# Kernel tuning notes

Hardware: AMD Instinct MI355X
Metric: run time of the kernel (lower is better)

Reference implementation:

```python
import jax, jax.numpy as jnp
import numpy as np
from functools import partial

D, H, O = 4, 64, 2  # input_dim, hidden_dim, output_dim


def lstm_layer(x, Wih, Whh, bih, bhh):
    """Single PyTorch-convention LSTM layer. x: [B,T,Din] -> [B,T,H].
    Gate order i,f,g,o; weights Wih:[4H,Din], Whh:[4H,H]."""
    B = x.shape[0]
    Hd = Whh.shape[1]
    # precompute input contribution for all timesteps (one big GEMM)
    xg = jnp.einsum('btd,gd->btg', x, Wih) + bih + bhh  # [B,T,4H]

    def step(carry, xg_t):
        h, c = carry
        g = xg_t + h @ Whh.T  # [B,4H]
        i, f, gg, o = jnp.split(g, 4, axis=-1)
        i = jax.nn.sigmoid(i)
        f = jax.nn.sigmoid(f)
        gg = jnp.tanh(gg)
        o = jax.nn.sigmoid(o)
        c = f * c + i * gg
        h = o * jnp.tanh(c)
        return (h, c), h

    h0 = jnp.zeros((B, Hd), x.dtype)
    c0 = jnp.zeros((B, Hd), x.dtype)
    (_, _), hs = jax.lax.scan(step, (h0, c0), jnp.swapaxes(xg, 0, 1))  # hs: [T,B,H]
    return jnp.swapaxes(hs, 0, 1)


def setup_inputs() -> dict:
    key = jax.random.key(0)
    ks = jax.random.split(key, 13)
    s_ih0 = 1.0 / np.sqrt(H)
    inp = {
        'x': jax.random.normal(ks[0], (16384, 100, D), jnp.float32),
        'W_ih0': jax.random.uniform(ks[1], (4 * H, D), jnp.float32, -s_ih0, s_ih0),
        'W_hh0': jax.random.uniform(ks[2], (4 * H, H), jnp.float32, -s_ih0, s_ih0),
        'b_ih0': jax.random.uniform(ks[3], (4 * H,), jnp.float32, -s_ih0, s_ih0),
        'b_hh0': jax.random.uniform(ks[4], (4 * H,), jnp.float32, -s_ih0, s_ih0),
        'W_ih1': jax.random.uniform(ks[5], (4 * H, H), jnp.float32, -s_ih0, s_ih0),
        'W_hh1': jax.random.uniform(ks[6], (4 * H, H), jnp.float32, -s_ih0, s_ih0),
        'b_ih1': jax.random.uniform(ks[7], (4 * H,), jnp.float32, -s_ih0, s_ih0),
        'b_hh1': jax.random.uniform(ks[8], (4 * H,), jnp.float32, -s_ih0, s_ih0),
        'gamma': jnp.ones((H,), jnp.float32),
        'beta': jnp.zeros((H,), jnp.float32),
        'W_fc': jax.random.uniform(ks[9], (O, H), jnp.float32, -s_ih0, s_ih0),
        'b_fc': jax.random.uniform(ks[10], (O,), jnp.float32, -s_ih0, s_ih0),
    }
    return inp


def reference(x, W_ih0, W_hh0, b_ih0, b_hh0, W_ih1, W_hh1, b_ih1, b_hh1,
              gamma, beta, W_fc, b_fc):
    h1 = lstm_layer(x, W_ih0, W_hh0, b_ih0, b_hh0)   # [B,T,H]
    h2 = lstm_layer(h1, W_ih1, W_hh1, b_ih1, b_hh1)  # [B,T,H] (dropout off: eval)
    last = h2[:, -1, :]                              # [B,H]
    mu = jnp.mean(last, axis=-1, keepdims=True)
    var = jnp.mean((last - mu) ** 2, axis=-1, keepdims=True)
    normed = (last - mu) * jax.lax.rsqrt(var + 1e-5) * gamma + beta
    return normed @ W_fc.T + b_fc                    # [B,2]
```

## Files before the change

kernel.cpp:

```cpp
#include <hip/hip_runtime.h>

#define TSTEPS 100
#define BC     16
#define NBLK   (16384/BC)

typedef __attribute__((ext_vector_type(8))) short bf16x8;
typedef __attribute__((ext_vector_type(4))) short s16x4;
typedef __attribute__((ext_vector_type(4))) float f32x4;
typedef __attribute__((ext_vector_type(2))) float f32x2;

#define WS_WHH0_U 0
#define WS_WIH1_U 16384
#define WS_WHH1_U 32768
#define WS_WIH0_U 49152
#define WS_B0_F   28672
#define WS_B1_F   28928
#define WS_XF_U   65536
#define WS_NEED   (131072 + (size_t)NBLK * TSTEPS * 64 * 2)

#define MFMA(A,B,C) __builtin_amdgcn_mfma_f32_16x16x32_bf16(A,B,C,0,0,0)
#define LOG2E 1.4426950408889634f
#define BF16_ONE ((short)0x3F80)

__device__ __forceinline__ unsigned short f2bf_rne(float f) {
    unsigned int u = __float_as_uint(f);
    u += 0x7fffu + ((u >> 16) & 1u);
    return (unsigned short)(u >> 16);
}
__device__ __forceinline__ unsigned short f2bf(float f) {
    return (unsigned short)((__float_as_uint(f) + 0x8000u) >> 16);
}
__device__ __forceinline__ f32x2 exp2v(f32x2 y) {
    return (f32x2){__builtin_amdgcn_exp2f(y.x), __builtin_amdgcn_exp2f(y.y)};
}
__device__ __forceinline__ f32x2 rcpv(f32x2 y) {
    return (f32x2){__builtin_amdgcn_rcpf(y.x), __builtin_amdgcn_rcpf(y.y)};
}

__device__ __forceinline__ f32x2 lstm_cell(f32x2 yi, f32x2 yf, f32x2 yg, f32x2 yo,
                                           f32x2& c) {
    const f32x2 one = {1.f, 1.f};
    const f32x2 L22 = {2.0f * LOG2E, 2.0f * LOG2E};
    const f32x2 Ei = exp2v(yi), Ef = exp2v(yf), Eg = exp2v(yg), Eo = exp2v(yo);
    const f32x2 t2 = Ef + one;
    const f32x2 t3 = Eg + one;
    const f32x2 u  = Ei * t3 + t3;
    const f32x2 n  = Eg * t2 - t2;
    const f32x2 R1 = rcpv(u * t2);
    c = (c * u + n) * R1;
    const f32x2 Ec = exp2v(c * L22);
    const f32x2 t6 = Ec + one;
    const f32x2 R2 = rcpv(Eo * t6 + t6);
    return Ec * R2 - R2;
}

__device__ __forceinline__ void bar_lds() {
    asm volatile("s_waitcnt lgkmcnt(0)\n\ts_barrier" ::: "memory");
}

__global__ void reorder_w(const float* __restrict__ Wih0, const float* __restrict__ Whh0,
                          const float* __restrict__ bih0, const float* __restrict__ bhh0,
                          const float* __restrict__ Wih1, const float* __restrict__ Whh1,
                          const float* __restrict__ bih1, const float* __restrict__ bhh1,
                          unsigned short* __restrict__ wsu, float* __restrict__ wsf)
{
    const int idx = blockIdx.x * 256 + threadIdx.x;
    if (idx < 16384) {
        const int j = idx & 7, lane = (idx >> 3) & 63, kc = (idx >> 9) & 1,
                  G = (idx >> 10) & 3, ug = (idx >> 12) & 3;
        const int row = G * 64 + ug * 16 + (lane & 15);
        const int k   = kc * 32 + (lane >> 4) * 8 + j;
        const float sc = (G == 2) ? (2.0f * LOG2E) : -LOG2E;
        wsu[WS_WHH0_U + idx] = f2bf_rne(sc * Whh0[row * 64 + k]);
        wsu[WS_WIH1_U + idx] = f2bf_rne(sc * Wih1[row * 64 + k]);
        wsu[WS_WHH1_U + idx] = f2bf_rne(sc * Whh1[row * 64 + k]);
    }
    if (idx < 8192) {
        const int j = idx & 7, lane = (idx >> 3) & 63, G = (idx >> 9) & 3, ug = (idx >> 11) & 3;
        const int row = G * 64 + ug * 16 + (lane & 15);
        const float sc = (G == 2) ? (2.0f * LOG2E) : -LOG2E;
        float v = 0.0f;
        if ((lane >> 4) == 0) {
            if (j < 4)       v = sc * Wih0[row * 4 + j];
            else if (j == 4) v = sc * (bih0[row] + bhh0[row]);
        }
        wsu[WS_WIH0_U + idx] = f2bf_rne(v);
    }
    if (idx < 256) {
        const int G = idx >> 6;
        const float sc = (G == 2) ? (2.0f * LOG2E) : -LOG2E;
        wsf[WS_B0_F + idx] = sc * (bih0[idx] + bhh0[idx]);
        wsf[WS_B1_F + idx] = sc * (bih1[idx] + bhh1[idx]);
    }
}

__global__ void prep_xfrag(const float* __restrict__ x, unsigned short* __restrict__ xf) {
    const int idx = blockIdx.x * 256 + threadIdx.x;
    const int t    = idx % TSTEPS;
    const int m    = (idx / TSTEPS) & 15;
    const int tile = idx / (TSTEPS * 16);
    const float4 v = *(const float4*)(x + ((size_t)(tile * 16 + m) * TSTEPS + t) * 4);
    const s16x4 o = {(short)f2bf_rne(v.x), (short)f2bf_rne(v.y),
                     (short)f2bf_rne(v.z), (short)f2bf_rne(v.w)};
    *(s16x4*)(xf + ((size_t)(tile * TSTEPS + t) * 16 + m) * 4) = o;
}

#define L0STEP(K, P)                                                             \
  {                                                                              \
    bf16x8 ax;                                                                   \
    if (XPRE) { U8 u_; u_.p.lo = xv; u_.p.hi = onev; ax = u_.v8; }               \
    else {                                                                       \
      ax = zfrag;                                                                \
      if (lg == 0) {                                                             \
        ax[0] = (short)f2bf_rne(xf4.x); ax[1] = (short)f2bf_rne(xf4.y);          \
        ax[2] = (short)f2bf_rne(xf4.z); ax[3] = (short)f2bf_rne(xf4.w);          \
        ax[4] = BF16_ONE;                                                        \
      }                                                                          \
    }                                                                            \
    f32x4 acc0[4];                                                               \
    _Pragma("unroll") for (int G = 0; G < 4; ++G) {                              \
      acc0[G] = MFMA(A0[0], Bhh0[G][0], zero4);                                  \
      acc0[G] = MFMA(A0[1], Bhh0[G][1], acc0[G]);                                \
      acc0[G] = MFMA(ax,    Bih0[G],    acc0[G]);                                \
    }                                                                            \
    if ((K) + 1 < TSTEPS) {                                                      \
      if (XPRE) xv  = *(const s16x4*)(xfp + ((K) + 1) * 64);                     \
      else      xf4 = *(const float4*)(xb + ((K) + 1) * 4);                      \
    }                                                                            \
    __builtin_amdgcn_s_setprio(1);                                               \
    _Pragma("unroll") for (int p = 0; p < 2; ++p) {                              \
      const f32x2 h = lstm_cell(                                                 \
        (f32x2){acc0[0][2*p], acc0[0][2*p+1]},                                   \
        (f32x2){acc0[1][2*p], acc0[1][2*p+1]},                                   \
        (f32x2){acc0[2][2*p], acc0[2][2*p+1]},                                   \
        (f32x2){acc0[3][2*p], acc0[3][2*p+1]}, c0v[p]);                          \
      *(unsigned short*)(HBc + ((P)<<11) + wadr[2*p])   = f2bf(h.x);             \
      *(unsigned short*)(HBc + ((P)<<11) + wadr[2*p+1]) = f2bf(h.y);             \
    }                                                                            \
    __builtin_amdgcn_s_setprio(0);                                               \
    bar_lds();                                                                   \
    A0[0] = *(const bf16x8*)(HBc + ((P)<<11) + rbase);                           \
    A0[1] = *(const bf16x8*)(HBc + ((P)<<11) + rbase + 1024);                    \
  }

#define L1STEP(J, P)                                                             \
  {                                                                              \
    f32x4 acc1[4];                                                               \
    _Pragma("unroll") for (int G = 0; G < 4; ++G) {                              \
      acc1[G] = MFMA(A0[0], Bih1[G][0], bV[G]);                                  \
      acc1[G] = MFMA(A0[1], Bih1[G][1], acc1[G]);                                \
      acc1[G] = MFMA(A1[0], Bhh1[G][0], acc1[G]);                                \
      acc1[G] = MFMA(A1[1], Bhh1[G][1], acc1[G]);                                \
    }                                                                            \
    __builtin_amdgcn_s_setprio(1);                                               \
    _Pragma("unroll") for (int p = 0; p < 2; ++p) {                              \
      const f32x2 h = lstm_cell(                                                 \
        (f32x2){acc1[0][2*p], acc1[0][2*p+1]},                                   \
        (f32x2){acc1[1][2*p], acc1[1][2*p+1]},                                   \
        (f32x2){acc1[2][2*p], acc1[2][2*p+1]},                                   \
        (f32x2){acc1[3][2*p], acc1[3][2*p+1]}, c1v[p]);                          \
      *(unsigned short*)(HBc + 4096 + ((P)<<11) + wadr[2*p])   = f2bf(h.x);      \
      *(unsigned short*)(HBc + 4096 + ((P)<<11) + wadr[2*p+1]) = f2bf(h.y);      \
    }                                                                            \
    __builtin_amdgcn_s_setprio(0);                                               \
    bar_lds();                                                                   \
    A0[0] = *(const bf16x8*)(HBc + (((P)^1)<<11) + rbase);                       \
    A0[1] = *(const bf16x8*)(HBc + (((P)^1)<<11) + rbase + 1024);                \
    A1[0] = *(const bf16x8*)(HBc + 4096 + ((P)<<11) + rbase);                    \
    A1[1] = *(const bf16x8*)(HBc + 4096 + ((P)<<11) + rbase + 1024);             \
  }

template<bool XPRE>
__global__ __launch_bounds__(512, 3) void lstm2_mfma(
    const float* __restrict__ x,
    const unsigned short* __restrict__ wsu, const float* __restrict__ wsf,
    const float* __restrict__ gam, const float* __restrict__ bet,
    const float* __restrict__ Wfc, const float* __restrict__ bfc,
    float* __restrict__ out)
{
    __shared__ __align__(16) unsigned short HB[4096];
    __shared__ float H1F[BC * 65];

    const int tid  = threadIdx.x;
    const int lane = tid & 63;
    const int wv   = __builtin_amdgcn_readfirstlane(tid >> 6);
    const int ug   = wv & 3;
    const int ln15 = lane & 15, lg = lane >> 4;
    const int bblk = blockIdx.x * BC;

    const int kcw = ug >> 1;
    const int lgc = ((ug & 1) << 1) + (ln15 >> 3);
    const unsigned wswz = (unsigned)((((lg >> 1) & 1) << 4) | (((ln15 >> 3) & 1) << 5));
    unsigned wadr[4];
    #pragma unroll
    for (int r = 0; r < 4; ++r)
        wadr[r] = ((unsigned)(kcw * 1024 + lgc * 256 + lg * 64 + r * 16 + (ln15 & 7) * 2)) ^ wswz;
    const unsigned rswz = (unsigned)((((lane >> 3) & 1) << 4) | (((lane >> 4) & 1) << 5));
    const unsigned rbase = ((unsigned)(lane * 16)) ^ rswz;
    char* const HBc = (char*)HB;

    const bf16x8 zfrag = {0,0,0,0,0,0,0,0};
    const f32x4 zero4 = {0.f, 0.f, 0.f, 0.f};
    const s16x4 onev = {BF16_ONE, 0, 0, 0};
    union U8 { bf16x8 v8; struct { s16x4 lo, hi; } p; };

    if (wv < 4) {
        bf16x8 Bhh0[4][2], Bih0[4];
        #pragma unroll
        for (int G = 0; G < 4; ++G) {
            #pragma unroll
            for (int kc = 0; kc < 2; ++kc)
                Bhh0[G][kc] = *(const bf16x8*)(wsu + WS_WHH0_U + (((ug*4+G)*2+kc)*512 + lane*8));
            Bih0[G] = *(const bf16x8*)(wsu + WS_WIH0_U + (ug*4+G)*512 + lane*8);
        }
        f32x2 c0v[2] = {{0.f,0.f},{0.f,0.f}};
        bf16x8 A0[2]; A0[0] = zfrag; A0[1] = zfrag;

        const unsigned short* xfp = wsu + WS_XF_U + (size_t)blockIdx.x * (TSTEPS * 64) + ln15 * 4;
        const float* xb = x + (size_t)(bblk + ln15) * (TSTEPS * 4);
        s16x4 xv = {0,0,0,0};
        float4 xf4;
        if (XPRE) xv = *(const s16x4*)(xfp);
        else      xf4 = *(const float4*)(xb);

        int k = 0;
        #pragma unroll 1
        for (int kb = 0; kb < TSTEPS / 2; ++kb) {
            L0STEP(k, 0);
            L0STEP(k + 1, 1);
            k += 2;
        }
        bar_lds();

        if (tid < BC) {
            const int b = tid;
            float hr[64];
            float mu = 0.f;
            #pragma unroll
            for (int q = 0; q < 64; ++q) { hr[q] = H1F[b * 65 + q]; mu += hr[q]; }
            mu *= (1.f / 64.f);
            float var = 0.f;
            #pragma unroll
            for (int q = 0; q < 64; ++q) { const float d = hr[q] - mu; var = fmaf(d, d, var); }
            var *= (1.f / 64.f);
            const float rs = rsqrtf(var + 1e-5f);
            float o0 = bfc[0], o1 = bfc[1];
            #pragma unroll
            for (int q = 0; q < 64; ++q) {
                const float nk = (hr[q] - mu) * rs * gam[q] + bet[q];
                o0 = fmaf(nk, Wfc[q],      o0);
                o1 = fmaf(nk, Wfc[64 + q], o1);
            }
            out[(size_t)(bblk + b) * 2 + 0] = o0;
            out[(size_t)(bblk + b) * 2 + 1] = o1;
        }
    } else {
        bf16x8 Bih1[4][2], Bhh1[4][2];
        #pragma unroll
        for (int G = 0; G < 4; ++G) {
            #pragma unroll
            for (int kc = 0; kc < 2; ++kc) {
                const int f = ((ug * 4 + G) * 2 + kc) * 512 + lane * 8;
                Bih1[G][kc] = *(const bf16x8*)(wsu + WS_WIH1_U + f);
                Bhh1[G][kc] = *(const bf16x8*)(wsu + WS_WHH1_U + f);
            }
        }
        f32x4 bV[4];
        #pragma unroll
        for (int G = 0; G < 4; ++G) {
            const float b = wsf[WS_B1_F + G * 64 + ug * 16 + ln15];
            bV[G] = (f32x4){b, b, b, b};
        }
        f32x2 c1v[2] = {{0.f,0.f},{0.f,0.f}};
        bf16x8 A0[2], A1[2];
        A1[0] = zfrag; A1[1] = zfrag;

        bar_lds();
        A0[0] = *(const bf16x8*)(HBc + rbase);
        A0[1] = *(const bf16x8*)(HBc + rbase + 1024);

        int j = 0;
        #pragma unroll 1
        for (int jb = 0; jb < (TSTEPS - 2) / 2; ++jb) {
            L1STEP(j, 0);
            L1STEP(j + 1, 1);
            j += 2;
        }
        L1STEP(98, 0);

        {
            f32x4 acc1[4];
            #pragma unroll
            for (int G = 0; G < 4; ++G) {
                acc1[G] = MFMA(A0[0], Bih1[G][0], bV[G]);
                acc1[G] = MFMA(A0[1], Bih1[G][1], acc1[G]);
                acc1[G] = MFMA(A1[0], Bhh1[G][0], acc1[G]);
                acc1[G] = MFMA(A1[1], Bhh1[G][1], acc1[G]);
            }
            __builtin_amdgcn_s_setprio(1);
            #pragma unroll
            for (int p = 0; p < 2; ++p) {
                const f32x2 h = lstm_cell(
                    (f32x2){acc1[0][2*p], acc1[0][2*p+1]},
                    (f32x2){acc1[1][2*p], acc1[1][2*p+1]},
                    (f32x2){acc1[2][2*p], acc1[2][2*p+1]},
                    (f32x2){acc1[3][2*p], acc1[3][2*p+1]}, c1v[p]);
                H1F[(lg * 4 + 2*p)     * 65 + ug * 16 + ln15] = h.x;
                H1F[(lg * 4 + 2*p + 1) * 65 + ug * 16 + ln15] = h.y;
            }
            __builtin_amdgcn_s_setprio(0);
        }
        bar_lds();
    }
}

extern "C" void kernel_launch(void* const* d_in, const int* in_sizes, int n_in,
                              void* d_out, int out_size, void* d_ws, size_t ws_size,
                              hipStream_t stream) {
    (void)in_sizes; (void)n_in; (void)out_size;
    const float* x    = (const float*)d_in[0];
    const float* Wih0 = (const float*)d_in[1];
    const float* Whh0 = (const float*)d_in[2];
    const float* bih0 = (const float*)d_in[3];
    const float* bhh0 = (const float*)d_in[4];
    const float* Wih1 = (const float*)d_in[5];
    const float* Whh1 = (const float*)d_in[6];
    const float* bih1 = (const float*)d_in[7];
    const float* bhh1 = (const float*)d_in[8];
    const float* gam  = (const float*)d_in[9];
    const float* bet  = (const float*)d_in[10];
    const float* Wfc  = (const float*)d_in[11];
    const float* bfc  = (const float*)d_in[12];
    unsigned short* wsu = (unsigned short*)d_ws;
    float*          wsf = (float*)d_ws;
    float* out = (float*)d_out;

    hipLaunchKernelGGL(reorder_w, dim3(96), dim3(256), 0, stream,
                       Wih0, Whh0, bih0, bhh0, Wih1, Whh1, bih1, bhh1, wsu, wsf);
    if (ws_size >= WS_NEED) {
        hipLaunchKernelGGL(prep_xfrag, dim3(NBLK * 16 * TSTEPS / 256), dim3(256), 0, stream,
                           x, wsu + WS_XF_U);
        hipLaunchKernelGGL((lstm2_mfma<true>), dim3(NBLK), dim3(512), 0, stream,
                           x, wsu, wsf, gam, bet, Wfc, bfc, out);
    } else {
        hipLaunchKernelGGL((lstm2_mfma<false>), dim3(NBLK), dim3(512), 0, stream,
                           x, wsu, wsf, gam, bet, Wfc, bfc, out);
    }
}
```

Baseline: 227.8 us.

## Process two 16-row batch tiles per block to halve barrier count per sample

Each block now handles 32 batch rows as two independent 16-row MFMA tiles. The two tiles share the weight fragments held in registers and the same per-step LDS barrier, so barrier and latency overhead is spread over twice the work. The LDS hidden-state buffer doubles and the grid halves. The s_setprio hints around the cell math are also removed. Register pressure rises (twice the accumulators, A fragments and cell states) under launch_bounds(512,3), which risks spills or lower occupancy, and only half as many blocks are available to fill the CUs.

```diff
diff --git a/kernel.cpp b/kernel.cpp
--- a/kernel.cpp
+++ b/kernel.cpp
@@ -1,7 +1,7 @@
 #include <hip/hip_runtime.h>
 
 #define TSTEPS 100
-#define BC     16
+#define BC     32
 #define NBLK   (16384/BC)
 
 typedef __attribute__((ext_vector_type(8))) short bf16x8;
@@ -16,7 +16,7 @@
 #define WS_B0_F   28672
 #define WS_B1_F   28928
 #define WS_XF_U   65536
-#define WS_NEED   (131072 + (size_t)NBLK * TSTEPS * 64 * 2)
+#define WS_NEED   (131072 + (size_t)1024 * TSTEPS * 64 * 2)
 
 #define MFMA(A,B,C) __builtin_amdgcn_mfma_f32_16x16x32_bf16(A,B,C,0,0,0)
 #define LOG2E 1.4426950408889634f
@@ -107,67 +107,77 @@
 
 #define L0STEP(K, P)                                                             \
   {                                                                              \
-    bf16x8 ax;                                                                   \
-    if (XPRE) { U8 u_; u_.p.lo = xv; u_.p.hi = onev; ax = u_.v8; }               \
-    else {                                                                       \
-      ax = zfrag;                                                                \
-      if (lg == 0) {                                                             \
-        ax[0] = (short)f2bf_rne(xf4.x); ax[1] = (short)f2bf_rne(xf4.y);          \
-        ax[2] = (short)f2bf_rne(xf4.z); ax[3] = (short)f2bf_rne(xf4.w);          \
-        ax[4] = BF16_ONE;                                                        \
+    bf16x8 ax[2];                                                                \
+    _Pragma("unroll") for (int mt = 0; mt < 2; ++mt) {                           \
+      if (XPRE) { U8 u_; u_.p.lo = xv[mt]; u_.p.hi = onev; ax[mt] = u_.v8; }     \
+      else {                                                                     \
+        ax[mt] = zfrag;                                                          \
+        if (lg == 0) {                                                           \
+          ax[mt][0] = (short)f2bf_rne(xf4[mt].x);                                \
+          ax[mt][1] = (short)f2bf_rne(xf4[mt].y);                                \
+          ax[mt][2] = (short)f2bf_rne(xf4[mt].z);                                \
+          ax[mt][3] = (short)f2bf_rne(xf4[mt].w);                                \
+          ax[mt][4] = BF16_ONE;                                                  \
+        }                                                                        \
       }                                                                          \
     }                                                                            \
-    f32x4 acc0[4];                                                               \
+    f32x4 acc0[2][4];                                                            \
+    _Pragma("unroll") for (int mt = 0; mt < 2; ++mt)                             \
     _Pragma("unroll") for (int G = 0; G < 4; ++G) {                              \
-      acc0[G] = MFMA(A0[0], Bhh0[G][0], zero4);                                  \
-      acc0[G] = MFMA(A0[1], Bhh0[G][1], acc0[G]);                                \
-      acc0[G] = MFMA(ax,    Bih0[G],    acc0[G]);                                \
+      acc0[mt][G] = MFMA(A0[mt][0], Bhh0[G][0], zero4);                          \
+      acc0[mt][G] = MFMA(A0[mt][1], Bhh0[G][1], acc0[mt][G]);                    \
+      acc0[mt][G] = MFMA(ax[mt],    Bih0[G],    acc0[mt][G]);                    \
     }                                                                            \
     if ((K) + 1 < TSTEPS) {                                                      \
-      if (XPRE) xv  = *(const s16x4*)(xfp + ((K) + 1) * 64);                     \
-      else      xf4 = *(const float4*)(xb + ((K) + 1) * 4);                      \
-    }                                                                            \
-    __builtin_amdgcn_s_setprio(1);                                               \
+      _Pragma("unroll") for (int mt = 0; mt < 2; ++mt) {                         \
+        if (XPRE) xv[mt]  = *(const s16x4*)(xfp[mt] + ((K) + 1) * 64);           \
+        else      xf4[mt] = *(const float4*)(xb[mt] + ((K) + 1) * 4);            \
+      }                                                                          \
+    }                                                                            \
+    _Pragma("unroll") for (int mt = 0; mt < 2; ++mt)                             \
     _Pragma("unroll") for (int p = 0; p < 2; ++p) {                              \
       const f32x2 h = lstm_cell(                                                 \
-        (f32x2){acc0[0][2*p], acc0[0][2*p+1]},                                   \
-        (f32x2){acc0[1][2*p], acc0[1][2*p+1]},                                   \
-        (f32x2){acc0[2][2*p], acc0[2][2*p+1]},                                   \
-        (f32x2){acc0[3][2*p], acc0[3][2*p+1]}, c0v[p]);                          \
-      *(unsigned short*)(HBc + ((P)<<11) + wadr[2*p])   = f2bf(h.x);             \
-      *(unsigned short*)(HBc + ((P)<<11) + wadr[2*p+1]) = f2bf(h.y);             \
-    }                                                                            \
-    __builtin_amdgcn_s_setprio(0);                                               \
+        (f32x2){acc0[mt][0][2*p], acc0[mt][0][2*p+1]},                           \
+        (f32x2){acc0[mt][1][2*p], acc0[mt][1][2*p+1]},                           \
+        (f32x2){acc0[mt][2][2*p], acc0[mt][2][2*p+1]},                           \
+        (f32x2){acc0[mt][3][2*p], acc0[mt][3][2*p+1]}, c0v[mt][p]);              \
+      *(unsigned short*)(HBc + ((P)<<12) + (mt<<11) + wadr[2*p])   = f2bf(h.x);  \
+      *(unsigned short*)(HBc + ((P)<<12) + (mt<<11) + wadr[2*p+1]) = f2bf(h.y);  \
+    }                                                                            \
     bar_lds();                                                                   \
-    A0[0] = *(const bf16x8*)(HBc + ((P)<<11) + rbase);                           \
-    A0[1] = *(const bf16x8*)(HBc + ((P)<<11) + rbase + 1024);                    \
+    _Pragma("unroll") for (int mt = 0; mt < 2; ++mt) {                           \
+      A0[mt][0] = *(const bf16x8*)(HBc + ((P)<<12) + (mt<<11) + rbase);          \
+      A0[mt][1] = *(const bf16x8*)(HBc + ((P)<<12) + (mt<<11) + rbase + 1024);   \
+    }                                                                            \
   }
 
 #define L1STEP(J, P)                                                             \
   {                                                                              \
-    f32x4 acc1[4];                                                               \
+    f32x4 acc1[2][4];                                                            \
+    _Pragma("unroll") for (int mt = 0; mt < 2; ++mt)                             \
     _Pragma("unroll") for (int G = 0; G < 4; ++G) {                              \
-      acc1[G] = MFMA(A0[0], Bih1[G][0], bV[G]);                                  \
-      acc1[G] = MFMA(A0[1], Bih1[G][1], acc1[G]);                                \
-      acc1[G] = MFMA(A1[0], Bhh1[G][0], acc1[G]);                                \
-      acc1[G] = MFMA(A1[1], Bhh1[G][1], acc1[G]);                                \
-    }                                                                            \
-    __builtin_amdgcn_s_setprio(1);                                               \
+      acc1[mt][G] = MFMA(A0[mt][0], Bih1[G][0], bV[G]);                          \
+      acc1[mt][G] = MFMA(A0[mt][1], Bih1[G][1], acc1[mt][G]);                    \
+      acc1[mt][G] = MFMA(A1[mt][0], Bhh1[G][0], acc1[mt][G]);                    \
+      acc1[mt][G] = MFMA(A1[mt][1], Bhh1[G][1], acc1[mt][G]);                    \
+    }                                                                            \
+    _Pragma("unroll") for (int mt = 0; mt < 2; ++mt)                             \
     _Pragma("unroll") for (int p = 0; p < 2; ++p) {                              \
       const f32x2 h = lstm_cell(                                                 \
-        (f32x2){acc1[0][2*p], acc1[0][2*p+1]},                                   \
-        (f32x2){acc1[1][2*p], acc1[1][2*p+1]},                                   \
-        (f32x2){acc1[2][2*p], acc1[2][2*p+1]},                                   \
-        (f32x2){acc1[3][2*p], acc1[3][2*p+1]}, c1v[p]);                          \
-      *(unsigned short*)(HBc + 4096 + ((P)<<11) + wadr[2*p])   = f2bf(h.x);      \
-      *(unsigned short*)(HBc + 4096 + ((P)<<11) + wadr[2*p+1]) = f2bf(h.y);      \
-    }                                                                            \
-    __builtin_amdgcn_s_setprio(0);                                               \
+        (f32x2){acc1[mt][0][2*p], acc1[mt][0][2*p+1]},                           \
+        (f32x2){acc1[mt][1][2*p], acc1[mt][1][2*p+1]},                           \
+        (f32x2){acc1[mt][2][2*p], acc1[mt][2][2*p+1]},                           \
+        (f32x2){acc1[mt][3][2*p], acc1[mt][3][2*p+1]}, c1v[mt][p]);              \
+      *(unsigned short*)(HBc + 8192 + ((P)<<12) + (mt<<11) + wadr[2*p])   = f2bf(h.x); \
+      *(unsigned short*)(HBc + 8192 + ((P)<<12) + (mt<<11) + wadr[2*p+1]) = f2bf(h.y); \
+    }                                                                            \
     bar_lds();                                                                   \
-    A0[0] = *(const bf16x8*)(HBc + (((P)^1)<<11) + rbase);                       \
-    A0[1] = *(const bf16x8*)(HBc + (((P)^1)<<11) + rbase + 1024);                \
-    A1[0] = *(const bf16x8*)(HBc + 4096 + ((P)<<11) + rbase);                    \
-    A1[1] = *(const bf16x8*)(HBc + 4096 + ((P)<<11) + rbase + 1024);             \
+    _Pragma("unroll") for (int mt = 0; mt < 2; ++mt) {                           \
+      A0[mt][0] = *(const bf16x8*)(HBc + (((P)^1)<<12) + (mt<<11) + rbase);      \
+      A0[mt][1] = *(const bf16x8*)(HBc + (((P)^1)<<12) + (mt<<11) + rbase + 1024); \
+      A1[mt][0] = *(const bf16x8*)(HBc + 8192 + ((P)<<12) + (mt<<11) + rbase);   \
+      A1[mt][1] = *(const bf16x8*)(HBc + 8192 + ((P)<<12) + (mt<<11) + rbase + 1024); \
+    }                                                                            \
   }
 
 template<bool XPRE>
@@ -178,7 +188,7 @@
     const float* __restrict__ Wfc, const float* __restrict__ bfc,
     float* __restrict__ out)
 {
-    __shared__ __align__(16) unsigned short HB[4096];
+    __shared__ __align__(16) unsigned short HB[8192];
     __shared__ float H1F[BC * 65];
 
     const int tid  = threadIdx.x;
@@ -213,15 +223,22 @@
                 Bhh0[G][kc] = *(const bf16x8*)(wsu + WS_WHH0_U + (((ug*4+G)*2+kc)*512 + lane*8));
             Bih0[G] = *(const bf16x8*)(wsu + WS_WIH0_U + (ug*4+G)*512 + lane*8);
         }
-        f32x2 c0v[2] = {{0.f,0.f},{0.f,0.f}};
-        bf16x8 A0[2]; A0[0] = zfrag; A0[1] = zfrag;
-
-        const unsigned short* xfp = wsu + WS_XF_U + (size_t)blockIdx.x * (TSTEPS * 64) + ln15 * 4;
-        const float* xb = x + (size_t)(bblk + ln15) * (TSTEPS * 4);
-        s16x4 xv = {0,0,0,0};
-        float4 xf4;
-        if (XPRE) xv = *(const s16x4*)(xfp);
-        else      xf4 = *(const float4*)(xb);
+        f32x2 c0v[2][2] = {{{0.f,0.f},{0.f,0.f}},{{0.f,0.f},{0.f,0.f}}};
+        bf16x8 A0[2][2];
+        #pragma unroll
+        for (int mt = 0; mt < 2; ++mt) { A0[mt][0] = zfrag; A0[mt][1] = zfrag; }
+
+        const unsigned short* xfp[2];
+        const float* xb[2];
+        s16x4 xv[2];
+        float4 xf4[2];
+        #pragma unroll
+        for (int mt = 0; mt < 2; ++mt) {
+            xfp[mt] = wsu + WS_XF_U + (size_t)(blockIdx.x * 2 + mt) * (TSTEPS * 64) + ln15 * 4;
+            xb[mt]  = x + (size_t)(bblk + mt * 16 + ln15) * (TSTEPS * 4);
+            if (XPRE) xv[mt] = *(const s16x4*)(xfp[mt]);
+            else      xf4[mt] = *(const float4*)(xb[mt]);
+        }
 
         int k = 0;
         #pragma unroll 1
@@ -271,13 +288,17 @@
             const float b = wsf[WS_B1_F + G * 64 + ug * 16 + ln15];
             bV[G] = (f32x4){b, b, b, b};
         }
-        f32x2 c1v[2] = {{0.f,0.f},{0.f,0.f}};
-        bf16x8 A0[2], A1[2];
-        A1[0] = zfrag; A1[1] = zfrag;
+        f32x2 c1v[2][2] = {{{0.f,0.f},{0.f,0.f}},{{0.f,0.f},{0.f,0.f}}};
+        bf16x8 A0[2][2], A1[2][2];
+        #pragma unroll
+        for (int mt = 0; mt < 2; ++mt) { A1[mt][0] = zfrag; A1[mt][1] = zfrag; }
 
         bar_lds();
-        A0[0] = *(const bf16x8*)(HBc + rbase);
-        A0[1] = *(const bf16x8*)(HBc + rbase + 1024);
+        #pragma unroll
+        for (int mt = 0; mt < 2; ++mt) {
+            A0[mt][0] = *(const bf16x8*)(HBc + (mt<<11) + rbase);
+            A0[mt][1] = *(const bf16x8*)(HBc + (mt<<11) + rbase + 1024);
+        }
 
         int j = 0;
         #pragma unroll 1
@@ -289,26 +310,28 @@
         L1STEP(98, 0);
 
         {
-            f32x4 acc1[4];
+            f32x4 acc1[2][4];
+            #pragma unroll
+            for (int mt = 0; mt < 2; ++mt)
             #pragma unroll
             for (int G = 0; G < 4; ++G) {
-                acc1[G] = MFMA(A0[0], Bih1[G][0], bV[G]);
-                acc1[G] = MFMA(A0[1], Bih1[G][1], acc1[G]);
-                acc1[G] = MFMA(A1[0], Bhh1[G][0], acc1[G]);
-                acc1[G] = MFMA(A1[1], Bhh1[G][1], acc1[G]);
+                acc1[mt][G] = MFMA(A0[mt][0], Bih1[G][0], bV[G]);
+                acc1[mt][G] = MFMA(A0[mt][1], Bih1[G][1], acc1[mt][G]);
+                acc1[mt][G] = MFMA(A1[mt][0], Bhh1[G][0], acc1[mt][G]);
+                acc1[mt][G] = MFMA(A1[mt][1], Bhh1[G][1], acc1[mt][G]);
             }
-            __builtin_amdgcn_s_setprio(1);
+            #pragma unroll
+            for (int mt = 0; mt < 2; ++mt)
             #pragma unroll
             for (int p = 0; p < 2; ++p) {
                 const f32x2 h = lstm_cell(
-                    (f32x2){acc1[0][2*p], acc1[0][2*p+1]},
-                    (f32x2){acc1[1][2*p], acc1[1][2*p+1]},
-                    (f32x2){acc1[2][2*p], acc1[2][2*p+1]},
-                    (f32x2){acc1[3][2*p], acc1[3][2*p+1]}, c1v[p]);
-                H1F[(lg * 4 + 2*p)     * 65 + ug * 16 + ln15] = h.x;
-                H1F[(lg * 4 + 2*p + 1) * 65 + ug * 16 + ln15] = h.y;
+                    (f32x2){acc1[mt][0][2*p], acc1[mt][0][2*p+1]},
+                    (f32x2){acc1[mt][1][2*p], acc1[mt][1][2*p+1]},
+                    (f32x2){acc1[mt][2][2*p], acc1[mt][2][2*p+1]},
+                    (f32x2){acc1[mt][3][2*p], acc1[mt][3][2*p+1]}, c1v[mt][p]);
+                H1F[(mt * 16 + lg * 4 + 2*p)     * 65 + ug * 16 + ln15] = h.x;
+                H1F[(mt * 16 + lg * 4 + 2*p + 1) * 65 + ug * 16 + ln15] = h.y;
             }
-            __builtin_amdgcn_s_setprio(0);
         }
         bar_lds();
     }
@@ -338,7 +361,7 @@
     hipLaunchKernelGGL(reorder_w, dim3(96), dim3(256), 0, stream,
                        Wih0, Whh0, bih0, bhh0, Wih1, Whh1, bih1, bhh1, wsu, wsf);
     if (ws_size >= WS_NEED) {
-        hipLaunchKernelGGL(prep_xfrag, dim3(NBLK * 16 * TSTEPS / 256), dim3(256), 0, stream,
+        hipLaunchKernelGGL(prep_xfrag, dim3(6400), dim3(256), 0, stream,
                            x, wsu + WS_XF_U);
         hipLaunchKernelGGL((lstm2_mfma<true>), dim3(NBLK), dim3(512), 0, stream,
                            x, wsu, wsf, gam, bet, Wfc, bfc, out);
```

After: 248.2 us. +9.0%, slower.
